# Kernel optimization log

Hardware: AMD Instinct MI355X
Metric: run time of the kernel (lower is better)

The kernel has to match this reference:

```python
import jax, jax.numpy as jnp
import numpy as np

T, B, D, H = 512, 64, 1024, 8
DH = D // H
LN_EPS = 1e-5


def setup_inputs() -> dict:
    ks = jax.random.split(jax.random.key(0), 12)
    s = 1.0 / np.sqrt(D)
    return {
        "x_real": jax.random.normal(ks[0], (T, B, D), jnp.float32),
        "x_imag": jax.random.normal(ks[1], (T, B, D), jnp.float32),
        "value_state": jnp.zeros((B, H, DH), jnp.float32),
        "t": jnp.arange(T, dtype=jnp.int64) if jax.config.jax_enable_x64 else jnp.arange(T, dtype=jnp.int32),
        # ComplexLinear input_proj (bias=True): weight layout [out, in] like torch
        "Wr_in": jax.random.normal(ks[2], (D, D), jnp.float32) * s,
        "Wi_in": jax.random.normal(ks[3], (D, D), jnp.float32) * s,
        "br_in": jax.random.normal(ks[4], (D,), jnp.float32) * 0.01,
        "bi_in": jax.random.normal(ks[5], (D,), jnp.float32) * 0.01,
        # LayerNorm affine
        "ln_gamma": jnp.ones((D,), jnp.float32),
        "ln_beta": jnp.zeros((D,), jnp.float32),
        # QKV linear (bias=False), torch layout [3D, D]
        "W_qkv": jax.random.normal(ks[6], (3 * D, D), jnp.float32) * s,
        # per-head EMA gate logits: log(alpha/(1-alpha)) with alpha=0.9
        "log_alpha": jnp.full((H,), float(np.log(0.9 / 0.1)), jnp.float32),
        # ComplexLinear output_proj (bias=False)
        "Wr_out": jax.random.normal(ks[7], (D, D), jnp.float32) * s,
        "Wi_out": jax.random.normal(ks[8], (D, D), jnp.float32) * s,
    }


def reference(x_real, x_imag, value_state, t, Wr_in, Wi_in, br_in, bi_in,
              ln_gamma, ln_beta, W_qkv, log_alpha, Wr_out, Wi_out):
    scale = jnp.asarray(np.sqrt(DH), x_real.dtype)
    alpha = jax.nn.sigmoid(log_alpha)[None, :, None]  # [1,H,1]

    def step(state, xs):
        xr, xi = xs  # [B,D] each
        # ComplexLinear input projection
        pr = xr @ Wr_in.T - xi @ Wi_in.T + br_in
        pi = xr @ Wi_in.T + xi @ Wr_in.T + bi_in
        xc = pr + pi
        # LayerNorm over last dim
        mu = xc.mean(-1, keepdims=True)
        var = ((xc - mu) ** 2).mean(-1, keepdims=True)
        xc = (xc - mu) * jax.lax.rsqrt(var + LN_EPS) * ln_gamma + ln_beta
        # QKV
        qkv = (xc @ W_qkv.T).reshape(-1, 3, H, DH)
        q, k, v = qkv[:, 0], qkv[:, 1], qkv[:, 2]  # [B,H,DH]
        # per-head sigmoid-gated EMA state update
        new_state = alpha * v + (1.0 - alpha) * state
        gate = jax.nn.sigmoid(jnp.sum(q * k, axis=-1, keepdims=True) / scale)  # [B,H,1]
        retrieved = (gate * new_state).reshape(-1, D)
        # ComplexLinear output projection with zero imaginary input
        return new_state, (retrieved @ Wr_out.T, retrieved @ Wi_out.T)

    final_state, (out_real, out_imag) = jax.lax.scan(step, value_state, (x_real, x_imag))
    return out_real, out_imag, final_state
```

## Files before the change

kernel.cpp:

```cpp
#include <hip/hip_runtime.h>
#include <stdint.h>

#define T_DIM 512
#define B_DIM 64
#define D_DIM 1024
#define H_DIM 8
#define DH_DIM 128
#define MROWS (T_DIM * B_DIM)

typedef unsigned short u16;
typedef __attribute__((ext_vector_type(8))) __bf16 bf16x8;
typedef __attribute__((ext_vector_type(4))) float f32x4;

__device__ __forceinline__ u16 f2bf(float f) {
  union { float f; uint32_t u; } v; v.f = f;
  uint32_t u = v.u;
  u += 0x7fffu + ((u >> 16) & 1u);
  return (u16)(u >> 16);
}
__device__ __forceinline__ float bf2f(u16 h) {
  union { uint32_t u; float f; } v; v.u = ((uint32_t)h) << 16;
  return v.f;
}

__device__ __forceinline__ void gload16(const void* g, void* l) {
  __builtin_amdgcn_global_load_lds(
      (const __attribute__((address_space(1))) uint32_t*)g,
      (__attribute__((address_space(3))) uint32_t*)l, 16, 0, 0);
}


__global__ void cast_bf16_kernel(const float* __restrict__ in, u16* __restrict__ out, size_t n8) {
  size_t i = (size_t)blockIdx.x * blockDim.x + threadIdx.x;
  const size_t stride = (size_t)gridDim.x * blockDim.x;
  for (; i < n8; i += stride) {
    const float4 a = ((const float4*)in)[i * 2];
    const float4 b = ((const float4*)in)[i * 2 + 1];
    union { u16 h[8]; uint4 u; } o;
    o.h[0] = f2bf(a.x); o.h[1] = f2bf(a.y); o.h[2] = f2bf(a.z); o.h[3] = f2bf(a.w);
    o.h[4] = f2bf(b.x); o.h[5] = f2bf(b.y); o.h[6] = f2bf(b.z); o.h[7] = f2bf(b.w);
    ((uint4*)out)[i] = o.u;
  }
}

__global__ void prep_wc_kernel(const float* __restrict__ Wr, const float* __restrict__ Wi,
                               u16* __restrict__ Wc) {
  const int idx = blockIdx.x * 256 + threadIdx.x;
  const int n = idx >> 11;
  const int k = idx & 2047;
  const int kk = k & 1023;
  const float a = Wr[n * 1024 + kk], b = Wi[n * 1024 + kk];
  Wc[idx] = f2bf(k < 1024 ? a + b : a - b);
}

__global__ void prep_bc_kernel(const float* __restrict__ br, const float* __restrict__ bi,
                               float* __restrict__ bc) {
  const int i = blockIdx.x * 256 + threadIdx.x;
  if (i < D_DIM) bc[i] = br[i] + bi[i];
}


template <int EPI>
__global__ __launch_bounds__(512, 2) void gemm256_kernel(
    const u16* __restrict__ A0, const u16* __restrict__ A1, int kSplit, int lda,
    const u16* __restrict__ Bw, int ldb,
    const float* __restrict__ bias,
    void* __restrict__ C0, void* __restrict__ C1, void* __restrict__ C2,
    int ldc, int K, int nColBlk)
{
  extern __shared__ u16 lds[];
  const int tid  = threadIdx.x;
  const int lane = tid & 63;
  const int w    = tid >> 6;
  const int wr   = w >> 2;
  const int wc   = w & 3;

  const int bid   = blockIdx.x;
  const int xcd   = bid & 7;
  const int local = bid >> 3;
  const int rowL  = local / nColBlk;
  const int colB  = local - rowL * nColBlk;
  const size_t rowBase = (size_t)(xcd * 16 + rowL) * 256;
  const size_t colBase = (size_t)colB * 256;

  f32x4 acc[8][4];
#pragma unroll
  for (int i = 0; i < 8; ++i)
#pragma unroll
    for (int j = 0; j < 4; ++j) acc[i][j] = (f32x4){0.f, 0.f, 0.f, 0.f};

  const int NT = K >> 6;

  auto stage = [&](int buf, int kh, int t) {
    const int kb = t * 64;
    const u16* Ab; int kc;
    if (kb < kSplit) { Ab = A0; kc = kb; } else { Ab = A1; kc = kb - kSplit; }
    u16* sA = lds + buf * 32768 + kh * 8192;
    u16* sB = lds + buf * 32768 + 16384 + kh * 8192;
#pragma unroll
    for (int i = 0; i < 2; ++i) {
      const int l = i * 512 + tid;
      const int r = l >> 2;
      const int ug = (l & 3) ^ (r & 3) ^ ((r >> 2) & 3);
      gload16(Ab + (rowBase + r) * (size_t)lda + (kc + kh * 32 + ug * 8), sA + l * 8);
      gload16(Bw + (colBase + r) * (size_t)ldb + (kb + kh * 32 + ug * 8), sB + l * 8);
    }
  };

  const int uo = (((lane >> 4) ^ (lane & 3) ^ ((lane >> 2) & 3)) << 3);
  const int la = lane & 15;

  auto computeH = [&](int buf, int ks) {
    const u16* sA = lds + buf * 32768 + ks * 8192;
    const u16* sB = lds + buf * 32768 + 16384 + ks * 8192;
#pragma unroll
    for (int q = 0; q < 4; ++q) {
      const int qm = q >> 1, qn = q & 1;
      const int ra = wr * 128 + qm * 64 + la;
      const int rb = wc * 64 + qn * 32 + la;
      bf16x8 a[4], b[2];
#pragma unroll
      for (int j = 0; j < 4; ++j) a[j] = *(const bf16x8*)(sA + (ra + j * 16) * 32 + uo);
#pragma unroll
      for (int j = 0; j < 2; ++j) b[j] = *(const bf16x8*)(sB + (rb + j * 16) * 32 + uo);
      __builtin_amdgcn_s_setprio(1);
#pragma unroll
      for (int j = 0; j < 4; ++j)
#pragma unroll
        for (int j2 = 0; j2 < 2; ++j2)
          acc[qm * 4 + j][qn * 2 + j2] =
              __builtin_amdgcn_mfma_f32_16x16x32_bf16(a[j], b[j2], acc[qm * 4 + j][qn * 2 + j2], 0, 0, 0);
      __builtin_amdgcn_s_setprio(0);
    }
  };

  stage(0, 0, 0);
  stage(0, 1, 0);
  stage(1, 0, 1);

  int cur = 0;
  for (int t = 0; t < NT; ++t, cur ^= 1) {
    asm volatile("s_waitcnt vmcnt(4)" ::: "memory");
    __builtin_amdgcn_sched_barrier(0);
    __builtin_amdgcn_s_barrier();
    __builtin_amdgcn_sched_barrier(0);
    if (t + 1 < NT) stage(cur ^ 1, 1, t + 1);
    computeH(cur, 0);
    __builtin_amdgcn_sched_barrier(0);
    __builtin_amdgcn_s_barrier();
    __builtin_amdgcn_sched_barrier(0);
    if (t + 2 < NT) stage(cur, 0, t + 2);
    computeH(cur, 1);
    __builtin_amdgcn_sched_barrier(0);
  }

  const int seg = (int)(colBase >> 10);
  const size_t colSeg = colBase & 1023;
  void* Cout;
  if (EPI == 3)      Cout = (seg == 0) ? C0 : (seg == 1) ? C1 : C2;
  else if (EPI == 2) Cout = (seg == 0) ? C0 : C1;
  else               Cout = C0;

#pragma unroll
  for (int mi = 0; mi < 8; ++mi)
#pragma unroll
    for (int ni = 0; ni < 4; ++ni) {
      const int cn = wc * 64 + ni * 16 + la;
      const float badd = (EPI == 1) ? bias[colBase + cn] : 0.0f;
      const size_t col = colSeg + cn;
#pragma unroll
      for (int r = 0; r < 4; ++r) {
        const size_t row = rowBase + wr * 128 + mi * 16 + (lane >> 4) * 4 + r;
        const float v = acc[mi][ni][r] + badd;
        if (EPI == 2) ((float*)Cout)[row * (size_t)ldc + col] = v;
        else          ((u16*)Cout)[row * (size_t)ldc + col] = f2bf(v);
      }
    }
}


__global__ __launch_bounds__(256) void ln_kernel(u16* __restrict__ xc,
    const float* __restrict__ gamma, const float* __restrict__ beta)
{
  const size_t row = blockIdx.x;
  u16* p = xc + row * D_DIM;
  const int tid = threadIdx.x;
  const int c = tid * 4;
  const uint2 raw = *(const uint2*)(p + c);
  const float v0 = bf2f((u16)(raw.x & 0xffff)), v1 = bf2f((u16)(raw.x >> 16));
  const float v2 = bf2f((u16)(raw.y & 0xffff)), v3 = bf2f((u16)(raw.y >> 16));
  float s = v0 + v1 + v2 + v3;
  float q = v0 * v0 + v1 * v1 + v2 * v2 + v3 * v3;
#pragma unroll
  for (int o = 32; o > 0; o >>= 1) { s += __shfl_xor(s, o); q += __shfl_xor(q, o); }
  __shared__ float red[8];
  if ((tid & 63) == 0) { red[(tid >> 6) * 2] = s; red[(tid >> 6) * 2 + 1] = q; }
  __syncthreads();
  s = red[0] + red[2] + red[4] + red[6];
  q = red[1] + red[3] + red[5] + red[7];
  const float mu = s * (1.0f / D_DIM);
  const float var = q * (1.0f / D_DIM) - mu * mu;
  const float rstd = 1.0f / sqrtf(var + 1e-5f);
  const float y0 = (v0 - mu) * rstd * gamma[c] + beta[c];
  const float y1 = (v1 - mu) * rstd * gamma[c + 1] + beta[c + 1];
  const float y2 = (v2 - mu) * rstd * gamma[c + 2] + beta[c + 2];
  const float y3 = (v3 - mu) * rstd * gamma[c + 3] + beta[c + 3];
  const uint32_t o0 = (uint32_t)f2bf(y0) | ((uint32_t)f2bf(y1) << 16);
  const uint32_t o1 = (uint32_t)f2bf(y2) | ((uint32_t)f2bf(y3) << 16);
  *(uint2*)(p + c) = make_uint2(o0, o1);
}


__global__ __launch_bounds__(256) void gate_kernel(
    const u16* __restrict__ Q, const u16* __restrict__ Kb, float* __restrict__ gate)
{
  const int gw = blockIdx.x * 4 + (threadIdx.x >> 6);
  const int lane = threadIdx.x & 63;
  const size_t row = (size_t)(gw >> 3);
  const int h = gw & 7;
  const size_t off = row * D_DIM + h * DH_DIM + lane * 2;
  const uint32_t qr = *(const uint32_t*)(Q + off);
  const uint32_t kr = *(const uint32_t*)(Kb + off);
  float d = bf2f((u16)(qr & 0xffff)) * bf2f((u16)(kr & 0xffff))
          + bf2f((u16)(qr >> 16))    * bf2f((u16)(kr >> 16));
#pragma unroll
  for (int o = 32; o > 0; o >>= 1) d += __shfl_xor(d, o);
  if (lane == 0) {
    const float x = d * 0.08838834764831845f;
    gate[gw] = 1.0f / (1.0f + expf(-x));
  }
}


__global__ __launch_bounds__(256) void scan_kernel(
    const u16* __restrict__ vb, const float* __restrict__ gate,
    const float* __restrict__ vstate, const float* __restrict__ log_alpha,
    u16* __restrict__ ret, float* __restrict__ fstate)
{
  const int gid = blockIdx.x * 256 + threadIdx.x;
  const int b = gid >> 10;
  const int c = gid & 1023;
  const int h = c >> 7;
  const float alpha = 1.0f / (1.0f + expf(-log_alpha[h]));
  const float oma = 1.0f - alpha;
  float state = vstate[gid];
  const u16* vp = vb + (size_t)b * D_DIM + c;
  u16* rp = ret + (size_t)b * D_DIM + c;
  const float* gp = gate + b * H_DIM + h;
#pragma unroll 4
  for (int t = 0; t < T_DIM; ++t) {
    const float v = bf2f(vp[(size_t)t * (B_DIM * D_DIM)]);
    const float g = gp[(size_t)t * (B_DIM * H_DIM)];
    state = alpha * v + oma * state;
    rp[(size_t)t * (B_DIM * D_DIM)] = f2bf(g * state);
  }
  fstate[gid] = state;
}


extern "C" void kernel_launch(void* const* d_in, const int* in_sizes, int n_in,
                              void* d_out, int out_size, void* d_ws, size_t ws_size,
                              hipStream_t stream) {
  const float* x_real      = (const float*)d_in[0];
  const float* x_imag      = (const float*)d_in[1];
  const float* value_state = (const float*)d_in[2];
  const float* Wr_in  = (const float*)d_in[4];
  const float* Wi_in  = (const float*)d_in[5];
  const float* br_in  = (const float*)d_in[6];
  const float* bi_in  = (const float*)d_in[7];
  const float* ln_g   = (const float*)d_in[8];
  const float* ln_b   = (const float*)d_in[9];
  const float* W_qkv  = (const float*)d_in[10];
  const float* log_alpha = (const float*)d_in[11];
  const float* Wr_out = (const float*)d_in[12];
  const float* Wi_out = (const float*)d_in[13];

  float* out_real = (float*)d_out;
  float* out_imag = out_real + (size_t)MROWS * D_DIM;
  float* fstate   = out_imag + (size_t)MROWS * D_DIM;

  u16* R0a = (u16*)d_out;
  u16* xc  = (u16*)((char*)d_out + (size_t)MROWS * D_DIM * 2);
  u16* Vb  = (u16*)out_imag;

  char* ws = (char*)d_ws;
  size_t off = 0;
  auto alloc = [&](size_t bytes) { void* p = ws + off; off += (bytes + 255) & ~(size_t)255; return p; };
  u16*   Wc    = (u16*)alloc((size_t)1024 * 2048 * 2);
  u16*   Wqkvb = (u16*)alloc((size_t)3072 * 1024 * 2);
  u16*   Wob   = (u16*)alloc((size_t)2048 * 1024 * 2);
  float* bc    = (float*)alloc((size_t)D_DIM * 4);
  u16*   R0b   = (u16*)alloc((size_t)MROWS * D_DIM * 2);
  float* gate  = (float*)alloc((size_t)MROWS * H_DIM * 4);

  const int LDSB = 131072;
  hipFuncSetAttribute((const void*)gemm256_kernel<1>, hipFuncAttributeMaxDynamicSharedMemorySize, LDSB);
  hipFuncSetAttribute((const void*)gemm256_kernel<2>, hipFuncAttributeMaxDynamicSharedMemorySize, LDSB);
  hipFuncSetAttribute((const void*)gemm256_kernel<3>, hipFuncAttributeMaxDynamicSharedMemorySize, LDSB);

  prep_wc_kernel<<<(1024 * 2048) / 256, 256, 0, stream>>>(Wr_in, Wi_in, Wc);
  prep_bc_kernel<<<4, 256, 0, stream>>>(br_in, bi_in, bc);
  cast_bf16_kernel<<<1536, 256, 0, stream>>>(W_qkv, Wqkvb, (size_t)3072 * 1024 / 8);
  cast_bf16_kernel<<<512, 256, 0, stream>>>(Wr_out, Wob, (size_t)1024 * 1024 / 8);
  cast_bf16_kernel<<<512, 256, 0, stream>>>(Wi_out, Wob + (size_t)1024 * 1024, (size_t)1024 * 1024 / 8);
  cast_bf16_kernel<<<4096, 256, 0, stream>>>(x_real, R0a, (size_t)MROWS * D_DIM / 8);
  cast_bf16_kernel<<<4096, 256, 0, stream>>>(x_imag, R0b, (size_t)MROWS * D_DIM / 8);

  gemm256_kernel<1><<<dim3(128 * 4), 512, LDSB, stream>>>(
      R0a, R0b, 1024, 1024, Wc, 2048, bc, xc, nullptr, nullptr, 1024, 2048, 4);
  ln_kernel<<<MROWS, 256, 0, stream>>>(xc, ln_g, ln_b);
  gemm256_kernel<3><<<dim3(128 * 12), 512, LDSB, stream>>>(
      xc, xc, 1024, 1024, Wqkvb, 1024, nullptr, R0a, R0b, Vb, 1024, 1024, 12);
  gate_kernel<<<(MROWS * H_DIM) / 4, 256, 0, stream>>>(R0a, R0b, gate);
  scan_kernel<<<(B_DIM * D_DIM) / 256, 256, 0, stream>>>(Vb, gate, value_state, log_alpha, R0b, fstate);
  gemm256_kernel<2><<<dim3(128 * 8), 512, LDSB, stream>>>(
      R0b, R0b, 1024, 1024, Wob, 1024, nullptr, out_real, out_imag, nullptr, 1024, 1024, 8);
}
```

Baseline: 797.2 us.

## Restructure GEMM main loop into eight barrier-fenced phases with split A/B staging

Replaces the two-half-step loop with an eight-phase schedule in which each phase reads its A fragments (and, every other phase, the B fragments), issues one A-only or B-only global-to-LDS load, then runs 16 MFMAs behind a barrier. B fragments now persist in registers across two phases, which cuts repeated LDS reads, and the global loads are spread more finely between compute phases. The cost is more workgroup barriers per K tile and a manually unrolled loop over pairs of tiles, which assumes NT is even.

```diff
diff --git a/kernel.cpp b/kernel.cpp
--- a/kernel.cpp
+++ b/kernel.cpp
@@ -59,6 +59,40 @@
   if (i < D_DIM) bc[i] = br[i] + bi[i];
 }
 
+
+template <int BUF, int KS, int QM, bool RB, bool VMW, typename F>
+__device__ __forceinline__ void phase_op(const u16* lds, f32x4 (&acc)[8][4],
+                                         bf16x8 (&bfr)[4], int wr, int wc, int la,
+                                         int puA, F&& stage) {
+  const u16* sA = lds + BUF * 32768 + KS * 8192;
+  bf16x8 afr[4];
+#pragma unroll
+  for (int j = 0; j < 4; ++j)
+    afr[j] = *(const bf16x8*)(sA + (wr * 128 + QM * 64 + j * 16 + la) * 32 + puA);
+  if (RB) {
+    const u16* sB = lds + BUF * 32768 + 16384 + KS * 8192;
+#pragma unroll
+    for (int ni = 0; ni < 4; ++ni)
+      bfr[ni] = *(const bf16x8*)(sB + (wc * 64 + ni * 16 + la) * 32 + puA);
+  }
+  stage();
+  __builtin_amdgcn_sched_barrier(0);
+  __builtin_amdgcn_s_barrier();
+  asm volatile("s_waitcnt lgkmcnt(0)" ::: "memory");
+  __builtin_amdgcn_sched_barrier(0);
+  __builtin_amdgcn_s_setprio(1);
+#pragma unroll
+  for (int mi = 0; mi < 4; ++mi)
+#pragma unroll
+    for (int ni = 0; ni < 4; ++ni)
+      acc[QM * 4 + mi][ni] =
+          __builtin_amdgcn_mfma_f32_16x16x32_bf16(afr[mi], bfr[ni], acc[QM * 4 + mi][ni], 0, 0, 0);
+  __builtin_amdgcn_s_setprio(0);
+  __builtin_amdgcn_sched_barrier(0);
+  if (VMW) asm volatile("s_waitcnt vmcnt(4)" ::: "memory");
+  __builtin_amdgcn_s_barrier();
+  __builtin_amdgcn_sched_barrier(0);
+}
 
 template <int EPI>
 __global__ __launch_bounds__(512, 2) void gemm256_kernel(
@@ -90,68 +124,54 @@
     for (int j = 0; j < 4; ++j) acc[i][j] = (f32x4){0.f, 0.f, 0.f, 0.f};
 
   const int NT = K >> 6;
-
-  auto stage = [&](int buf, int kh, int t) {
+  const int la = lane & 15;
+  const int g  = lane >> 4;
+  const int puA = ((g ^ (la & 3) ^ ((la >> 2) & 3)) << 3);
+
+  auto stageA = [&](int buf, int ks, int t) {
+    if (t >= NT) return;
     const int kb = t * 64;
     const u16* Ab; int kc;
     if (kb < kSplit) { Ab = A0; kc = kb; } else { Ab = A1; kc = kb - kSplit; }
-    u16* sA = lds + buf * 32768 + kh * 8192;
-    u16* sB = lds + buf * 32768 + 16384 + kh * 8192;
-#pragma unroll
-    for (int i = 0; i < 2; ++i) {
-      const int l = i * 512 + tid;
-      const int r = l >> 2;
-      const int ug = (l & 3) ^ (r & 3) ^ ((r >> 2) & 3);
-      gload16(Ab + (rowBase + r) * (size_t)lda + (kc + kh * 32 + ug * 8), sA + l * 8);
-      gload16(Bw + (colBase + r) * (size_t)ldb + (kb + kh * 32 + ug * 8), sB + l * 8);
+    u16* dst = lds + buf * 32768 + ks * 8192;
+#pragma unroll
+    for (int i2 = 0; i2 < 2; ++i2) {
+      const int l = i2 * 512 + tid, r = l >> 2, p = l & 3;
+      const int lu = p ^ (r & 3) ^ ((r >> 2) & 3);
+      gload16(Ab + (rowBase + r) * (size_t)lda + kc + ks * 32 + lu * 8, dst + l * 8);
     }
   };
-
-  const int uo = (((lane >> 4) ^ (lane & 3) ^ ((lane >> 2) & 3)) << 3);
-  const int la = lane & 15;
-
-  auto computeH = [&](int buf, int ks) {
-    const u16* sA = lds + buf * 32768 + ks * 8192;
-    const u16* sB = lds + buf * 32768 + 16384 + ks * 8192;
-#pragma unroll
-    for (int q = 0; q < 4; ++q) {
-      const int qm = q >> 1, qn = q & 1;
-      const int ra = wr * 128 + qm * 64 + la;
-      const int rb = wc * 64 + qn * 32 + la;
-      bf16x8 a[4], b[2];
-#pragma unroll
-      for (int j = 0; j < 4; ++j) a[j] = *(const bf16x8*)(sA + (ra + j * 16) * 32 + uo);
-#pragma unroll
-      for (int j = 0; j < 2; ++j) b[j] = *(const bf16x8*)(sB + (rb + j * 16) * 32 + uo);
-      __builtin_amdgcn_s_setprio(1);
-#pragma unroll
-      for (int j = 0; j < 4; ++j)
-#pragma unroll
-        for (int j2 = 0; j2 < 2; ++j2)
-          acc[qm * 4 + j][qn * 2 + j2] =
-              __builtin_amdgcn_mfma_f32_16x16x32_bf16(a[j], b[j2], acc[qm * 4 + j][qn * 2 + j2], 0, 0, 0);
-      __builtin_amdgcn_s_setprio(0);
+  auto stageB = [&](int buf, int ks, int t) {
+    if (t >= NT) return;
+    const int kb = t * 64;
+    u16* dst = lds + buf * 32768 + 16384 + ks * 8192;
+#pragma unroll
+    for (int i2 = 0; i2 < 2; ++i2) {
+      const int l = i2 * 512 + tid, r = l >> 2, p = l & 3;
+      const int lu = p ^ (r & 3) ^ ((r >> 2) & 3);
+      gload16(Bw + (colBase + r) * (size_t)ldb + kb + ks * 32 + lu * 8, dst + l * 8);
     }
   };
 
-  stage(0, 0, 0);
-  stage(0, 1, 0);
-  stage(1, 0, 1);
-
-  int cur = 0;
-  for (int t = 0; t < NT; ++t, cur ^= 1) {
-    asm volatile("s_waitcnt vmcnt(4)" ::: "memory");
-    __builtin_amdgcn_sched_barrier(0);
-    __builtin_amdgcn_s_barrier();
-    __builtin_amdgcn_sched_barrier(0);
-    if (t + 1 < NT) stage(cur ^ 1, 1, t + 1);
-    computeH(cur, 0);
-    __builtin_amdgcn_sched_barrier(0);
-    __builtin_amdgcn_s_barrier();
-    __builtin_amdgcn_sched_barrier(0);
-    if (t + 2 < NT) stage(cur, 0, t + 2);
-    computeH(cur, 1);
-    __builtin_amdgcn_sched_barrier(0);
+  stageA(0, 0, 0); stageB(0, 0, 0); stageA(0, 1, 0); stageB(0, 1, 0);
+  stageA(1, 0, 1); stageB(1, 0, 1);
+  asm volatile("s_waitcnt vmcnt(4)" ::: "memory");
+  __builtin_amdgcn_sched_barrier(0);
+  __builtin_amdgcn_s_barrier();
+  __builtin_amdgcn_sched_barrier(0);
+
+  bf16x8 bfr[4];
+  const int NIT = NT >> 1;
+  for (int i = 0; i < NIT; ++i) {
+    const int u = 2 * i, v = 2 * i + 1;
+    phase_op<0, 0, 0, true , false>(lds, acc, bfr, wr, wc, la, puA, [&] { stageA(1, 1, v); });
+    phase_op<0, 0, 1, false, false>(lds, acc, bfr, wr, wc, la, puA, [&] { stageB(1, 1, v); });
+    phase_op<0, 1, 0, true , false>(lds, acc, bfr, wr, wc, la, puA, [&] { stageA(0, 0, u + 2); });
+    phase_op<0, 1, 1, false, true >(lds, acc, bfr, wr, wc, la, puA, [&] { stageB(0, 0, u + 2); });
+    phase_op<1, 0, 0, true , false>(lds, acc, bfr, wr, wc, la, puA, [&] { stageA(0, 1, u + 2); });
+    phase_op<1, 0, 1, false, false>(lds, acc, bfr, wr, wc, la, puA, [&] { stageB(0, 1, u + 2); });
+    phase_op<1, 1, 0, true , false>(lds, acc, bfr, wr, wc, la, puA, [&] { stageA(1, 0, v + 2); });
+    phase_op<1, 1, 1, false, true >(lds, acc, bfr, wr, wc, la, puA, [&] { stageB(1, 0, v + 2); });
   }
 
   const int seg = (int)(colBase >> 10);
```

Measured after the change: 764.4 us. 4.1% less time.
